# Kernel tuning notes

Hardware: AMD Instinct MI355X
Metric: run time of the kernel (lower is better)

## Reference

```python
import jax, jax.numpy as jnp
from jax import lax
import numpy as np

HPDF = np.array([-0.0544158422, 0.3128715909, -0.6756307363, 0.5853546837,
                 0.0158291053, -0.284015543, -0.0004724846, 0.1287474266,
                 0.017369301, -0.0440882539, -0.0139810279, 0.008746094,
                 0.004870353, -0.0003917404, -0.0006754494, -0.0001174768],
                dtype=np.float32)


def setup_inputs() -> dict:
    key = jax.random.key(0)
    x = jax.random.normal(key, (8, 3, 512, 512), dtype=jnp.float32)
    hpdf = jnp.asarray(HPDF)
    return {"x": x, "hpdf": hpdf}


def _dwconv(inp, k2d, channels):
    # depthwise valid cross-correlation (matches F.conv2d with groups=C)
    n = k2d.shape[0]
    k = jnp.broadcast_to(k2d[None, None], (channels, 1, n, n))
    return lax.conv_general_dilated(
        inp, k, window_strides=(1, 1), padding='VALID',
        dimension_numbers=('NCHW', 'OIHW', 'NCHW'),
        feature_group_count=channels)


def reference(x, hpdf):
    B, C, H, W = x.shape
    n = hpdf.shape[0]  # 16 taps
    sign = (-1.0) ** jnp.arange(n, dtype=jnp.float32)
    lpdf = sign * hpdf[::-1]
    filters = [jnp.outer(lpdf, hpdf),   # LH
               jnp.outer(hpdf, lpdf),   # HL
               jnp.outer(hpdf, hpdf)]   # HH
    pad = n - 1  # 15
    xp = jnp.pad(x, ((0, 0), (0, 0), (pad, pad), (pad, pad)), mode='reflect')

    xis = []
    for f in filters:
        R = _dwconv(xp, f, C)                       # [B,C,H+15,W+15]
        xi = _dwconv(jnp.abs(R), jnp.abs(f[::-1, ::-1]), C)  # [B,C,H,W]
        # filter side length 16 is even -> roll by 1 on both spatial dims
        xi = jnp.roll(jnp.roll(xi, 1, axis=-1), 1, axis=-2)
        xis.append(xi)

    xi_stack = jnp.stack(xis, axis=0)               # [3,B,C,H,W]
    # p = -1: rho = (sum xi^p)^(-1/p) = sum(1/xi)
    rho = jnp.sum(1.0 / xi_stack, axis=0)
    wet = 1e10
    rho = jnp.minimum(rho, wet)
    rho = jnp.where(jnp.isnan(rho), wet, rho)
    mn = rho.min(axis=(-2, -1), keepdims=True)
    mx = rho.max(axis=(-2, -1), keepdims=True)
    rho = (rho - mn) / (mx - mn + 1e-8)
    score = jax.nn.sigmoid(1.0 - rho)
    return x * score
```

## Files before the change

### kernel.cpp

```cpp
#include <hip/hip_runtime.h>
#include <math.h>

#define IMG   512
#define NIMG  24
#define XST   72
#define TST   104
#define RST   56
#define UST   88

#define SA_TL  0
#define SA_TH  4992
#define SA_X   9984
#define SA_R   9984
#define RSZ    4480
#define SA_U   0
#define USZ    2816
#define SA_FT  22112
#define POOLSZ 23424

typedef _Float16 v8h __attribute__((ext_vector_type(8)));
typedef float    v4f __attribute__((ext_vector_type(4)));

__device__ __forceinline__ v8h load8(const _Float16* p) {
    union { uint4 u; v8h h; } c;
    c.u = *(const uint4*)p;
    return c.h;
}

__device__ __forceinline__ unsigned pkrtz(float a, float b) {
    union { __fp16 __attribute__((ext_vector_type(2))) v; unsigned u; } c;
    c.v = __builtin_amdgcn_cvt_pkrtz(a, b);
    return c.u;
}

__device__ __forceinline__ void store4(_Float16* p, v4f a) {
    union { _Float16 h[4]; uint2 u; } c;
    c.h[0] = (_Float16)a[0]; c.h[1] = (_Float16)a[1];
    c.h[2] = (_Float16)a[2]; c.h[3] = (_Float16)a[3];
    *(uint2*)p = c.u;
}

__device__ __forceinline__ void store4abs(_Float16* p, v4f a) {
    union { _Float16 h[4]; uint2 u; } c;
    c.h[0] = (_Float16)fabsf(a[0]); c.h[1] = (_Float16)fabsf(a[1]);
    c.h[2] = (_Float16)fabsf(a[2]); c.h[3] = (_Float16)fabsf(a[3]);
    *(uint2*)p = c.u;
}

__device__ __forceinline__ unsigned short f2bf(float f) {
    unsigned b = __float_as_uint(f);
    b = (b + 0x7fffu + ((b >> 16) & 1u)) >> 16;
    return (unsigned short)b;
}

__device__ __forceinline__ int refl(int g) {
    return g < 0 ? -g : (g >= IMG ? 2 * IMG - 2 - g : g);
}

__global__ __launch_bounds__(512, 6) void stego_stage1(
    const float* __restrict__ x, const float* __restrict__ hpdf,
    unsigned short* __restrict__ rho_out, float2* __restrict__ bmm)
{
    __shared__ __align__(16) _Float16 pool[POOLSZ];
    __shared__ float red[16];

    const int tid = threadIdx.x;
    const int lane = tid & 63;
    const int wid = __builtin_amdgcn_readfirstlane(tid >> 6);
    const int n16 = lane & 15, quad = lane >> 4;

    const int blk = blockIdx.x;
    const int xcd = blk & 7;
    const int grp = blk >> 3;
    const int img = xcd + ((grp >> 7) << 3);
    const int tl  = grp & 127;
    const int Oi = (tl >> 4) << 6;
    const int Oj = (tl & 15) << 5;
    const float* ximg = x + (size_t)img * (IMG * IMG);

    for (int e = tid; e < 1312; e += 512) {
        const int mode = e / 328;
        const int rem  = e - mode * 328;
        const int tap  = (rem >> 3) + (rem & 7) - 16;
        float v = 0.f;
        if (tap >= 0 && tap <= 15) {
            int idx = (mode == 0 || mode == 2) ? tap : 15 - tap;
            float c = hpdf[idx];
            if (mode == 1 && (tap & 1)) c = -c;
            if (mode >= 2) c = fabsf(c);
            v = c;
        }
        pool[SA_FT + e] = (_Float16)v;
    }

    {
        const int cg = tid & 15, row0 = tid >> 4;
        const int c0 = Oj - 16 + 4 * cg;
        _Float16* dst = pool + SA_X + row0 * XST + 4 * cg;
        if (Oi >= 15 && Oi <= 433 && Oj >= 16 && Oj <= 464) {
            const float* src = ximg + (size_t)(Oi - 15 + row0) * IMG + c0;
            #pragma unroll
            for (int k = 0; k < 3; ++k) {
                const int row = row0 + (k << 5);
                uint2 pv = make_uint2(0u, 0u);
                if (row < 94) {
                    float4 xv = *(const float4*)(src + (size_t)(k << 5) * IMG);
                    pv.x = pkrtz(xv.x, xv.y);
                    pv.y = pkrtz(xv.z, xv.w);
                }
                *(uint2*)(dst + (size_t)(k << 5) * XST) = pv;
            }
        } else {
            const int gj0 = refl(c0),     gj1 = refl(c0 + 1);
            const int gj2 = refl(c0 + 2), gj3 = refl(c0 + 3);
            #pragma unroll
            for (int k = 0; k < 3; ++k) {
                const int row = row0 + (k << 5);
                uint2 pv = make_uint2(0u, 0u);
                if (row < 94) {
                    const float* rsrc = ximg + (size_t)refl(Oi - 15 + row) * IMG;
                    pv.x = pkrtz(rsrc[gj0], rsrc[gj1]);
                    pv.y = pkrtz(rsrc[gj2], rsrc[gj3]);
                }
                *(uint2*)(dst + (size_t)(k << 5) * XST) = pv;
            }
        }
    }
    __syncthreads();

    v8h band[4], bandA[2];
    {
        const int sA = 16 + quad * 8 - n16;
        #pragma unroll
        for (int m = 0; m < 4; ++m)
            band[m] = load8(pool + SA_FT + (m * 41 + sA) * 8);
        #pragma unroll
        for (int m = 0; m < 2; ++m)
            bandA[m] = load8(pool + SA_FT + (m * 41 + sA - 1) * 8);
    }

    {
        const int laneX = n16 * XST + quad * 8;
        const int laneT = n16 * TST + quad * 4;
        const int u0 = wid, u1 = wid + 8, u2 = wid + 16;
        const int lo0 = (u0 % 6) * 16 * XST + (u0 / 6) * 16;
        const int lo1 = (u1 % 6) * 16 * XST + (u1 / 6) * 16;
        const int lo2 = (u2 % 6) * 16 * XST + (u2 / 6) * 16;
        const int so0 = (u0 / 6) * 16 * TST + (u0 % 6) * 16;
        const int so1 = (u1 / 6) * 16 * TST + (u1 % 6) * 16;
        const int so2 = (u2 / 6) * 16 * TST + (u2 % 6) * 16;
        v8h a0 = load8(pool + SA_X + lo0 + laneX);
        v8h a1 = load8(pool + SA_X + lo1 + laneX);
        v8h a2;
        if (wid < 2) a2 = load8(pool + SA_X + lo2 + laneX);
        const v4f z = {0.f, 0.f, 0.f, 0.f};
        v4f cL0 = __builtin_amdgcn_mfma_f32_16x16x32_f16(a0, bandA[1], z, 0, 0, 0);
        v4f cH0 = __builtin_amdgcn_mfma_f32_16x16x32_f16(a0, bandA[0], z, 0, 0, 0);
        v4f cL1 = __builtin_amdgcn_mfma_f32_16x16x32_f16(a1, bandA[1], z, 0, 0, 0);
        v4f cH1 = __builtin_amdgcn_mfma_f32_16x16x32_f16(a1, bandA[0], z, 0, 0, 0);
        store4(pool + SA_TL + so0 + laneT, cL0);
        store4(pool + SA_TH + so0 + laneT, cH0);
        store4(pool + SA_TL + so1 + laneT, cL1);
        store4(pool + SA_TH + so1 + laneT, cH1);
        if (wid < 2) {
            v4f cL2 = __builtin_amdgcn_mfma_f32_16x16x32_f16(a2, bandA[1], z, 0, 0, 0);
            v4f cH2 = __builtin_amdgcn_mfma_f32_16x16x32_f16(a2, bandA[0], z, 0, 0, 0);
            store4(pool + SA_TL + so2 + laneT, cL2);
            store4(pool + SA_TH + so2 + laneT, cH2);
        }
    }
    __syncthreads();

    {
        const int laneTB = n16 * TST + quad * 8;
        const int laneR  = n16 * RST + quad * 4;
        int ulo[6], uso[6], uf[6];
        #pragma unroll
        for (int k = 0; k < 6; ++k) {
            const int v = (k < 5) ? (wid + 8 * k) : (40 + wid);
            const int f = v / 15, rem = v - 15 * f;
            const int i0 = (rem % 5) * 16, c0 = (rem / 5) * 16;
            ulo[k] = (f == 0 ? SA_TL : SA_TH) + c0 * TST + i0;
            uso[k] = SA_R + f * RSZ + i0 * RST + c0;
            uf[k]  = f;
        }
        v8h aB[6];
        #pragma unroll
        for (int k = 0; k < 6; ++k)
            if (k < 5 || wid < 5) aB[k] = load8(pool + ulo[k] + laneTB);
        #pragma unroll
        for (int k = 0; k < 6; ++k)
            if (k < 5 || wid < 5) {
                const v4f z = {0.f, 0.f, 0.f, 0.f};
                v4f acc = __builtin_amdgcn_mfma_f32_16x16x32_f16(
                    aB[k], (uf[k] == 1) ? band[1] : band[0], z, 0, 0, 0);
                store4abs(pool + uso[k] + laneR, acc);
            }
    }
    __syncthreads();

    {
        const int laneRC = n16 * RST + quad * 8;
        const int laneU  = n16 * UST + quad * 4;
        int ulo[4], uso[4], uf[4];
        #pragma unroll
        for (int k = 0; k < 4; ++k) {
            const int v = (k < 3) ? (wid + 8 * k) : (24 + wid);
            const int f = v / 10, rem = v - 10 * f;
            const int i0 = (rem % 5) * 16, j0 = (rem / 5) * 16;
            ulo[k] = SA_R + f * RSZ + i0 * RST + j0;
            uso[k] = SA_U + f * USZ + j0 * UST + i0;
            uf[k]  = f;
        }
        v8h aC[4];
        #pragma unroll
        for (int k = 0; k < 4; ++k)
            if (k < 3 || wid < 6) aC[k] = load8(pool + ulo[k] + laneRC);
        #pragma unroll
        for (int k = 0; k < 4; ++k)
            if (k < 3 || wid < 6) {
                const v4f z = {0.f, 0.f, 0.f, 0.f};
                v4f acc = __builtin_amdgcn_mfma_f32_16x16x32_f16(
                    aC[k], (uf[k] == 0) ? band[2] : band[3], z, 0, 0, 0);
                store4(pool + uso[k] + laneU, acc);
            }
    }
    __syncthreads();

    float rho[4];
    {
        const int i0 = (wid & 3) * 16, c0 = (wid >> 2) * 16;
        const int laneUD = n16 * UST + quad * 8;
        const int ub = c0 * UST + i0 + laneUD;
        v8h d0 = load8(pool + SA_U + 0 * USZ + ub);
        v8h d1 = load8(pool + SA_U + 1 * USZ + ub);
        v8h d2 = load8(pool + SA_U + 2 * USZ + ub);
        const v4f z = {0.f, 0.f, 0.f, 0.f};
        v4f x0 = __builtin_amdgcn_mfma_f32_16x16x32_f16(d0, band[3], z, 0, 0, 0);
        v4f x1 = __builtin_amdgcn_mfma_f32_16x16x32_f16(d1, band[2], z, 0, 0, 0);
        v4f x2 = __builtin_amdgcn_mfma_f32_16x16x32_f16(d2, band[3], z, 0, 0, 0);
        #pragma unroll
        for (int r = 0; r < 4; ++r)
            rho[r] = __builtin_amdgcn_rcpf(x0[r]) + __builtin_amdgcn_rcpf(x1[r])
                   + __builtin_amdgcn_rcpf(x2[r]);
    }

    const size_t rbase = (size_t)img * (IMG * IMG);
    const int i_nat = Oi + (wid & 3) * 16 + n16;
    const int jb = Oj + ((wid >> 2) << 4) + quad * 4;
    float lmin = 1e38f, lmax = 0.f;
    unsigned pk0, pk1;
    {
        unsigned short b[4];
        #pragma unroll
        for (int r = 0; r < 4; ++r) {
            float v = rho[r];
            v = isnan(v) ? 1e10f : fminf(v, 1e10f);
            b[r] = f2bf(v);
            float rq = __uint_as_float((unsigned)b[r] << 16);
            lmin = fminf(lmin, rq);
            lmax = fmaxf(lmax, rq);
        }
        pk0 = (unsigned)b[0] | ((unsigned)b[1] << 16);
        pk1 = (unsigned)b[2] | ((unsigned)b[3] << 16);
    }
    *(uint2*)(rho_out + rbase + ((size_t)i_nat << 9) + jb) = make_uint2(pk0, pk1);

    #pragma unroll
    for (int off = 32; off >= 1; off >>= 1) {
        lmin = fminf(lmin, __shfl_xor(lmin, off));
        lmax = fmaxf(lmax, __shfl_xor(lmax, off));
    }
    if ((tid & 63) == 0) { red[wid] = lmin; red[8 + wid] = lmax; }
    __syncthreads();
    if (tid == 0) {
        float m0 = red[0], m1 = red[8];
        #pragma unroll
        for (int k = 1; k < 8; ++k) { m0 = fminf(m0, red[k]); m1 = fmaxf(m1, red[8 + k]); }
        bmm[(img << 7) + tl] = make_float2(m0, m1);
    }
}

__global__ __launch_bounds__(256) void stego_stage2(
    const float* __restrict__ x, const unsigned short* __restrict__ rho,
    const float2* __restrict__ bmm, float* __restrict__ out)
{
    __shared__ float sred[8];
    const int tid = threadIdx.x;
    const int lane = tid & 63;

    const int blk = blockIdx.x;
    const int xcd = blk & 7, grp = blk >> 3;
    const int img = xcd + ((grp >> 7) << 3);
    const int chunk = grp & 127;
    const int t = (img << 15) + (chunk << 8) + tid;

    float lmn = 1e38f, lmx = 0.f;
    if (tid < 128) { float2 p = bmm[(img << 7) + tid]; lmn = p.x; lmx = p.y; }
    #pragma unroll
    for (int off = 32; off >= 1; off >>= 1) {
        lmn = fminf(lmn, __shfl_xor(lmn, off));
        lmx = fmaxf(lmx, __shfl_xor(lmx, off));
    }
    if (tid < 128 && (tid & 63) == 0) { sred[tid >> 6] = lmn; sred[4 + (tid >> 6)] = lmx; }
    __syncthreads();
    const float mn = fminf(sred[0], sred[1]);
    const float mx = fmaxf(sred[4], sred[5]);
    const float inv = __builtin_amdgcn_rcpf(mx - mn + 1e-8f);

    const int i = (t >> 6) & 511;
    const int rrow = (i - 1) & 511;
    const size_t rb_off = ((size_t)img << 18) + ((size_t)rrow << 9) + ((size_t)lane << 3);
    uint4 rb = *(const uint4*)(rho + rb_off);
    unsigned ru[4] = {rb.x, rb.y, rb.z, rb.w};
    float f7 = __uint_as_float(ru[3] & 0xffff0000u);
    float r[8];
    r[0] = __shfl(f7, (lane + 63) & 63);
    r[1] = __uint_as_float(ru[0] << 16);
    r[2] = __uint_as_float(ru[0] & 0xffff0000u);
    r[3] = __uint_as_float(ru[1] << 16);
    r[4] = __uint_as_float(ru[1] & 0xffff0000u);
    r[5] = __uint_as_float(ru[2] << 16);
    r[6] = __uint_as_float(ru[2] & 0xffff0000u);
    r[7] = __uint_as_float(ru[3] << 16);

    const size_t base = (size_t)t << 3;
    const float* xrow = x + base;
    float4 xa = *(const float4*)xrow;
    float4 xb = *(const float4*)(xrow + 4);
    float xs[8] = {xa.x, xa.y, xa.z, xa.w, xb.x, xb.y, xb.z, xb.w};
    float os[8];
    #pragma unroll
    for (int k = 0; k < 8; ++k) {
        float rn = (r[k] - mn) * inv;
        os[k] = xs[k] * __builtin_amdgcn_rcpf(1.f + __expf(rn - 1.f));
    }
    float* orow = out + base;
    *(float4*)orow       = make_float4(os[0], os[1], os[2], os[3]);
    *(float4*)(orow + 4) = make_float4(os[4], os[5], os[6], os[7]);
}

extern "C" void kernel_launch(void* const* d_in, const int* in_sizes, int n_in,
                              void* d_out, int out_size, void* d_ws, size_t ws_size,
                              hipStream_t stream) {
    const float* x    = (const float*)d_in[0];
    const float* hpdf = (const float*)d_in[1];
    float* out = (float*)d_out;

    unsigned short* rho = (unsigned short*)d_ws;
    float2* bmm = (float2*)((char*)d_ws + (size_t)NIMG * IMG * IMG * 2);

    hipLaunchKernelGGL(stego_stage1, dim3(NIMG * 128), dim3(512), 0, stream,
                       x, hpdf, rho, bmm);
    hipLaunchKernelGGL(stego_stage2, dim3(NIMG * 128), dim3(256), 0, stream,
                       x, rho, bmm, out);
}
```

Measured before the change: 109.9 us.

## Fuse both stages into one persistent cooperative kernel with a grid sync

Merges the rho computation stage and the normalize/sigmoid stage into a single persistent cooperative kernel. Blocks loop over tiles, a grid-wide barrier replaces the kernel boundary, and the filter band fragments are loaded into registers once per block instead of once per tile. This removes the second launch and the per-tile filter setup. The costs are a grid-wide sync, a grid capped at 3 blocks per CU (768 blocks), and occupancy and tail effects in the persistent loops. It falls back to the two-kernel path if the cooperative launch fails.

```diff
diff --git a/kernel.cpp b/kernel.cpp
--- a/kernel.cpp
+++ b/kernel.cpp
@@ -1,5 +1,8 @@
 #include <hip/hip_runtime.h>
+#include <hip/hip_cooperative_groups.h>
 #include <math.h>
+
+namespace cg = cooperative_groups;
 
 #define IMG   512
 #define NIMG  24
@@ -57,9 +60,10 @@
     return g < 0 ? -g : (g >= IMG ? 2 * IMG - 2 - g : g);
 }
 
-__global__ __launch_bounds__(512, 6) void stego_stage1(
+__global__ __launch_bounds__(512, 6) void stego_fused(
     const float* __restrict__ x, const float* __restrict__ hpdf,
-    unsigned short* __restrict__ rho_out, float2* __restrict__ bmm)
+    unsigned short* __restrict__ rho_out, float2* __restrict__ bmm,
+    float* __restrict__ out)
 {
     __shared__ __align__(16) _Float16 pool[POOLSZ];
     __shared__ float red[16];
@@ -68,15 +72,6 @@
     const int lane = tid & 63;
     const int wid = __builtin_amdgcn_readfirstlane(tid >> 6);
     const int n16 = lane & 15, quad = lane >> 4;
-
-    const int blk = blockIdx.x;
-    const int xcd = blk & 7;
-    const int grp = blk >> 3;
-    const int img = xcd + ((grp >> 7) << 3);
-    const int tl  = grp & 127;
-    const int Oi = (tl >> 4) << 6;
-    const int Oj = (tl & 15) << 5;
-    const float* ximg = x + (size_t)img * (IMG * IMG);
 
     for (int e = tid; e < 1312; e += 512) {
         const int mode = e / 328;
@@ -92,11 +87,302 @@
         }
         pool[SA_FT + e] = (_Float16)v;
     }
-
-    {
-        const int cg = tid & 15, row0 = tid >> 4;
-        const int c0 = Oj - 16 + 4 * cg;
-        _Float16* dst = pool + SA_X + row0 * XST + 4 * cg;
+    __syncthreads();
+
+    v8h band[4], bandA[2];
+    {
+        const int sA = 16 + quad * 8 - n16;
+        #pragma unroll
+        for (int m = 0; m < 4; ++m)
+            band[m] = load8(pool + SA_FT + (m * 41 + sA) * 8);
+        #pragma unroll
+        for (int m = 0; m < 2; ++m)
+            bandA[m] = load8(pool + SA_FT + (m * 41 + sA - 1) * 8);
+    }
+
+    for (int T = blockIdx.x; T < NIMG * 128; T += gridDim.x) {
+        const int c = T & 7, s = T >> 3;
+        const int img = c + ((s >> 7) << 3);
+        const int tl  = s & 127;
+        const int Oi = (tl >> 4) << 6;
+        const int Oj = (tl & 15) << 5;
+        const float* ximg = x + (size_t)img * (IMG * IMG);
+
+        {
+            const int cg2 = tid & 15, row0 = tid >> 4;
+            const int c0 = Oj - 16 + 4 * cg2;
+            _Float16* dst = pool + SA_X + row0 * XST + 4 * cg2;
+            if (Oi >= 15 && Oi <= 433 && Oj >= 16 && Oj <= 464) {
+                const float* src = ximg + (size_t)(Oi - 15 + row0) * IMG + c0;
+                #pragma unroll
+                for (int k = 0; k < 3; ++k) {
+                    const int row = row0 + (k << 5);
+                    uint2 pv = make_uint2(0u, 0u);
+                    if (row < 94) {
+                        float4 xv = *(const float4*)(src + (size_t)(k << 5) * IMG);
+                        pv.x = pkrtz(xv.x, xv.y);
+                        pv.y = pkrtz(xv.z, xv.w);
+                    }
+                    *(uint2*)(dst + (size_t)(k << 5) * XST) = pv;
+                }
+            } else {
+                const int gj0 = refl(c0),     gj1 = refl(c0 + 1);
+                const int gj2 = refl(c0 + 2), gj3 = refl(c0 + 3);
+                #pragma unroll
+                for (int k = 0; k < 3; ++k) {
+                    const int row = row0 + (k << 5);
+                    uint2 pv = make_uint2(0u, 0u);
+                    if (row < 94) {
+                        const float* rsrc = ximg + (size_t)refl(Oi - 15 + row) * IMG;
+                        pv.x = pkrtz(rsrc[gj0], rsrc[gj1]);
+                        pv.y = pkrtz(rsrc[gj2], rsrc[gj3]);
+                    }
+                    *(uint2*)(dst + (size_t)(k << 5) * XST) = pv;
+                }
+            }
+        }
+        __syncthreads();
+
+        {
+            const int laneX = n16 * XST + quad * 8;
+            const int laneT = n16 * TST + quad * 4;
+            const int u0 = wid, u1 = wid + 8, u2 = wid + 16;
+            const int lo0 = (u0 % 6) * 16 * XST + (u0 / 6) * 16;
+            const int lo1 = (u1 % 6) * 16 * XST + (u1 / 6) * 16;
+            const int lo2 = (u2 % 6) * 16 * XST + (u2 / 6) * 16;
+            const int so0 = (u0 / 6) * 16 * TST + (u0 % 6) * 16;
+            const int so1 = (u1 / 6) * 16 * TST + (u1 % 6) * 16;
+            const int so2 = (u2 / 6) * 16 * TST + (u2 % 6) * 16;
+            v8h a0 = load8(pool + SA_X + lo0 + laneX);
+            v8h a1 = load8(pool + SA_X + lo1 + laneX);
+            v8h a2;
+            if (wid < 2) a2 = load8(pool + SA_X + lo2 + laneX);
+            const v4f z = {0.f, 0.f, 0.f, 0.f};
+            v4f cL0 = __builtin_amdgcn_mfma_f32_16x16x32_f16(a0, bandA[1], z, 0, 0, 0);
+            v4f cH0 = __builtin_amdgcn_mfma_f32_16x16x32_f16(a0, bandA[0], z, 0, 0, 0);
+            v4f cL1 = __builtin_amdgcn_mfma_f32_16x16x32_f16(a1, bandA[1], z, 0, 0, 0);
+            v4f cH1 = __builtin_amdgcn_mfma_f32_16x16x32_f16(a1, bandA[0], z, 0, 0, 0);
+            store4(pool + SA_TL + so0 + laneT, cL0);
+            store4(pool + SA_TH + so0 + laneT, cH0);
+            store4(pool + SA_TL + so1 + laneT, cL1);
+            store4(pool + SA_TH + so1 + laneT, cH1);
+            if (wid < 2) {
+                v4f cL2 = __builtin_amdgcn_mfma_f32_16x16x32_f16(a2, bandA[1], z, 0, 0, 0);
+                v4f cH2 = __builtin_amdgcn_mfma_f32_16x16x32_f16(a2, bandA[0], z, 0, 0, 0);
+                store4(pool + SA_TL + so2 + laneT, cL2);
+                store4(pool + SA_TH + so2 + laneT, cH2);
+            }
+        }
+        __syncthreads();
+
+        {
+            const int laneTB = n16 * TST + quad * 8;
+            const int laneR  = n16 * RST + quad * 4;
+            int ulo[6], uso[6], uf[6];
+            #pragma unroll
+            for (int k = 0; k < 6; ++k) {
+                const int v = (k < 5) ? (wid + 8 * k) : (40 + wid);
+                const int f = v / 15, rem = v - 15 * f;
+                const int i0 = (rem % 5) * 16, c0 = (rem / 5) * 16;
+                ulo[k] = (f == 0 ? SA_TL : SA_TH) + c0 * TST + i0;
+                uso[k] = SA_R + f * RSZ + i0 * RST + c0;
+                uf[k]  = f;
+            }
+            v8h aB[6];
+            #pragma unroll
+            for (int k = 0; k < 6; ++k)
+                if (k < 5 || wid < 5) aB[k] = load8(pool + ulo[k] + laneTB);
+            #pragma unroll
+            for (int k = 0; k < 6; ++k)
+                if (k < 5 || wid < 5) {
+                    const v4f z = {0.f, 0.f, 0.f, 0.f};
+                    v4f acc = __builtin_amdgcn_mfma_f32_16x16x32_f16(
+                        aB[k], (uf[k] == 1) ? band[1] : band[0], z, 0, 0, 0);
+                    store4abs(pool + uso[k] + laneR, acc);
+                }
+        }
+        __syncthreads();
+
+        {
+            const int laneRC = n16 * RST + quad * 8;
+            const int laneU  = n16 * UST + quad * 4;
+            int ulo[4], uso[4], uf[4];
+            #pragma unroll
+            for (int k = 0; k < 4; ++k) {
+                const int v = (k < 3) ? (wid + 8 * k) : (24 + wid);
+                const int f = v / 10, rem = v - 10 * f;
+                const int i0 = (rem % 5) * 16, j0 = (rem / 5) * 16;
+                ulo[k] = SA_R + f * RSZ + i0 * RST + j0;
+                uso[k] = SA_U + f * USZ + j0 * UST + i0;
+                uf[k]  = f;
+            }
+            v8h aC[4];
+            #pragma unroll
+            for (int k = 0; k < 4; ++k)
+                if (k < 3 || wid < 6) aC[k] = load8(pool + ulo[k] + laneRC);
+            #pragma unroll
+            for (int k = 0; k < 4; ++k)
+                if (k < 3 || wid < 6) {
+                    const v4f z = {0.f, 0.f, 0.f, 0.f};
+                    v4f acc = __builtin_amdgcn_mfma_f32_16x16x32_f16(
+                        aC[k], (uf[k] == 0) ? band[2] : band[3], z, 0, 0, 0);
+                    store4(pool + uso[k] + laneU, acc);
+                }
+        }
+        __syncthreads();
+
+        float rho[4];
+        {
+            const int i0 = (wid & 3) * 16, c0 = (wid >> 2) * 16;
+            const int laneUD = n16 * UST + quad * 8;
+            const int ub = c0 * UST + i0 + laneUD;
+            v8h d0 = load8(pool + SA_U + 0 * USZ + ub);
+            v8h d1 = load8(pool + SA_U + 1 * USZ + ub);
+            v8h d2 = load8(pool + SA_U + 2 * USZ + ub);
+            const v4f z = {0.f, 0.f, 0.f, 0.f};
+            v4f x0 = __builtin_amdgcn_mfma_f32_16x16x32_f16(d0, band[3], z, 0, 0, 0);
+            v4f x1 = __builtin_amdgcn_mfma_f32_16x16x32_f16(d1, band[2], z, 0, 0, 0);
+            v4f x2 = __builtin_amdgcn_mfma_f32_16x16x32_f16(d2, band[3], z, 0, 0, 0);
+            #pragma unroll
+            for (int r = 0; r < 4; ++r)
+                rho[r] = __builtin_amdgcn_rcpf(x0[r]) + __builtin_amdgcn_rcpf(x1[r])
+                       + __builtin_amdgcn_rcpf(x2[r]);
+        }
+
+        const size_t rbase = (size_t)img * (IMG * IMG);
+        const int i_nat = Oi + (wid & 3) * 16 + n16;
+        const int jb = Oj + ((wid >> 2) << 4) + quad * 4;
+        float lmin = 1e38f, lmax = 0.f;
+        unsigned pk0, pk1;
+        {
+            unsigned short b[4];
+            #pragma unroll
+            for (int r = 0; r < 4; ++r) {
+                float v = rho[r];
+                v = isnan(v) ? 1e10f : fminf(v, 1e10f);
+                b[r] = f2bf(v);
+                float rq = __uint_as_float((unsigned)b[r] << 16);
+                lmin = fminf(lmin, rq);
+                lmax = fmaxf(lmax, rq);
+            }
+            pk0 = (unsigned)b[0] | ((unsigned)b[1] << 16);
+            pk1 = (unsigned)b[2] | ((unsigned)b[3] << 16);
+        }
+        *(uint2*)(rho_out + rbase + ((size_t)i_nat << 9) + jb) = make_uint2(pk0, pk1);
+
+        #pragma unroll
+        for (int off = 32; off >= 1; off >>= 1) {
+            lmin = fminf(lmin, __shfl_xor(lmin, off));
+            lmax = fmaxf(lmax, __shfl_xor(lmax, off));
+        }
+        if ((tid & 63) == 0) { red[wid] = lmin; red[8 + wid] = lmax; }
+        __syncthreads();
+        if (tid == 0) {
+            float m0 = red[0], m1 = red[8];
+            #pragma unroll
+            for (int k = 1; k < 8; ++k) { m0 = fminf(m0, red[k]); m1 = fmaxf(m1, red[8 + k]); }
+            bmm[(img << 7) + tl] = make_float2(m0, m1);
+        }
+    }
+
+    __threadfence();
+    cg::this_grid().sync();
+
+    for (int T2 = blockIdx.x; T2 < 768; T2 += gridDim.x) {
+        const int c2 = T2 & 7, s2 = T2 >> 3;
+        const int img2 = c2 + ((s2 >> 5) << 3);
+        const int q2 = s2 & 31;
+
+        float lmn = 1e38f, lmx = 0.f;
+        if (tid < 128) { float2 p = bmm[(img2 << 7) + tid]; lmn = p.x; lmx = p.y; }
+        #pragma unroll
+        for (int off = 32; off >= 1; off >>= 1) {
+            lmn = fminf(lmn, __shfl_xor(lmn, off));
+            lmx = fmaxf(lmx, __shfl_xor(lmx, off));
+        }
+        if (tid < 128 && (tid & 63) == 0) { red[tid >> 6] = lmn; red[4 + (tid >> 6)] = lmx; }
+        __syncthreads();
+        const float mn = fminf(red[0], red[1]);
+        const float mx = fmaxf(red[4], red[5]);
+        const float inv = __builtin_amdgcn_rcpf(mx - mn + 1e-8f);
+
+        const size_t ib = (size_t)img2 << 18;
+        #pragma unroll
+        for (int rr = 0; rr < 2; ++rr) {
+            const int row = (q2 << 4) + (wid << 1) + rr;
+            const int rrow = (row - 1) & 511;
+            uint4 rb = *(const uint4*)(rho_out + ib + ((size_t)rrow << 9) + (lane << 3));
+            unsigned ru[4] = {rb.x, rb.y, rb.z, rb.w};
+            float f7 = __uint_as_float(ru[3] & 0xffff0000u);
+            float r[8];
+            r[0] = __shfl(f7, (lane + 63) & 63);
+            r[1] = __uint_as_float(ru[0] << 16);
+            r[2] = __uint_as_float(ru[0] & 0xffff0000u);
+            r[3] = __uint_as_float(ru[1] << 16);
+            r[4] = __uint_as_float(ru[1] & 0xffff0000u);
+            r[5] = __uint_as_float(ru[2] << 16);
+            r[6] = __uint_as_float(ru[2] & 0xffff0000u);
+            r[7] = __uint_as_float(ru[3] << 16);
+
+            const size_t pbase = ib + ((size_t)row << 9) + (lane << 3);
+            const float* xrow = x + pbase;
+            float4 xa = *(const float4*)xrow;
+            float4 xb = *(const float4*)(xrow + 4);
+            float xs[8] = {xa.x, xa.y, xa.z, xa.w, xb.x, xb.y, xb.z, xb.w};
+            float os[8];
+            #pragma unroll
+            for (int k = 0; k < 8; ++k) {
+                float rn = (r[k] - mn) * inv;
+                os[k] = xs[k] * __builtin_amdgcn_rcpf(1.f + __expf(rn - 1.f));
+            }
+            float* orow = out + pbase;
+            *(float4*)orow       = make_float4(os[0], os[1], os[2], os[3]);
+            *(float4*)(orow + 4) = make_float4(os[4], os[5], os[6], os[7]);
+        }
+        __syncthreads();
+    }
+}
+
+__global__ __launch_bounds__(512, 6) void stego_stage1(
+    const float* __restrict__ x, const float* __restrict__ hpdf,
+    unsigned short* __restrict__ rho_out, float2* __restrict__ bmm)
+{
+    __shared__ __align__(16) _Float16 pool[POOLSZ];
+    __shared__ float red[16];
+
+    const int tid = threadIdx.x;
+    const int lane = tid & 63;
+    const int wid = __builtin_amdgcn_readfirstlane(tid >> 6);
+    const int n16 = lane & 15, quad = lane >> 4;
+
+    const int blk = blockIdx.x;
+    const int xcd = blk & 7;
+    const int grp = blk >> 3;
+    const int img = xcd + ((grp >> 7) << 3);
+    const int tl  = grp & 127;
+    const int Oi = (tl >> 4) << 6;
+    const int Oj = (tl & 15) << 5;
+    const float* ximg = x + (size_t)img * (IMG * IMG);
+
+    for (int e = tid; e < 1312; e += 512) {
+        const int mode = e / 328;
+        const int rem  = e - mode * 328;
+        const int tap  = (rem >> 3) + (rem & 7) - 16;
+        float v = 0.f;
+        if (tap >= 0 && tap <= 15) {
+            int idx = (mode == 0 || mode == 2) ? tap : 15 - tap;
+            float c = hpdf[idx];
+            if (mode == 1 && (tap & 1)) c = -c;
+            if (mode >= 2) c = fabsf(c);
+            v = c;
+        }
+        pool[SA_FT + e] = (_Float16)v;
+    }
+
+    {
+        const int cg2 = tid & 15, row0 = tid >> 4;
+        const int c0 = Oj - 16 + 4 * cg2;
+        _Float16* dst = pool + SA_X + row0 * XST + 4 * cg2;
         if (Oi >= 15 && Oi <= 433 && Oj >= 16 && Oj <= 464) {
             const float* src = ximg + (size_t)(Oi - 15 + row0) * IMG + c0;
             #pragma unroll
@@ -350,8 +636,22 @@
     unsigned short* rho = (unsigned short*)d_ws;
     float2* bmm = (float2*)((char*)d_ws + (size_t)NIMG * IMG * IMG * 2);
 
-    hipLaunchKernelGGL(stego_stage1, dim3(NIMG * 128), dim3(512), 0, stream,
-                       x, hpdf, rho, bmm);
-    hipLaunchKernelGGL(stego_stage2, dim3(NIMG * 128), dim3(256), 0, stream,
-                       x, rho, bmm, out);
-}
+    int nb = 0;
+    hipError_t e = hipOccupancyMaxActiveBlocksPerMultiprocessor(
+        &nb, reinterpret_cast<const void*>(stego_fused), 512, 0);
+    bool done = false;
+    if (e == hipSuccess && nb >= 1) {
+        if (nb > 3) nb = 3;
+        dim3 grid(256 * nb);
+        void* args[] = {(void*)&x, (void*)&hpdf, (void*)&rho, (void*)&bmm, (void*)&out};
+        e = hipLaunchCooperativeKernel(reinterpret_cast<const void*>(stego_fused),
+                                       grid, dim3(512), args, 0, stream);
+        done = (e == hipSuccess);
+    }
+    if (!done) {
+        hipLaunchKernelGGL(stego_stage1, dim3(NIMG * 128), dim3(512), 0, stream,
+                           x, hpdf, rho, bmm);
+        hipLaunchKernelGGL(stego_stage2, dim3(NIMG * 128), dim3(256), 0, stream,
+                           x, rho, bmm, out);
+    }
+}
```

Result: slower. 279.8 us (+154.5%).
